# Kernel optimization log

Measured on AMD Instinct MI355X. Metric: run time of the kernel, lower is better.

## Reference

```python
import jax, jax.numpy as jnp
import numpy as np

N, E, B = 50000, 200000, 512
F0, H1, C2, EMB = 78, 10, 128, 128
SEQ, VOCAB, NF, KW = 1000, 26, 32, 8
LOUT = EMB - KW + 1  # 121


def setup_inputs() -> dict:
    key = jax.random.key(0)
    ks = jax.random.split(key, 20)
    nrm = lambda k, s: jax.random.normal(k, s, jnp.float32) * 0.05
    return dict(
        x=jax.random.normal(ks[0], (N, F0), jnp.float32),
        edge_index=jax.random.randint(ks[1], (2, E), 0, N),
        batch=(jnp.arange(N) * B) // N,  # balanced sorted node->graph ids, all segments non-empty
        target=jax.random.randint(ks[2], (B, SEQ), 0, VOCAB),
        W1=nrm(ks[3], (F0, H1 * F0)), a_src1=nrm(ks[4], (H1, F0)), a_dst1=nrm(ks[5], (H1, F0)), b1=jnp.zeros((H1 * F0,), jnp.float32),
        W2=nrm(ks[6], (H1 * F0, C2)), a_src2=nrm(ks[7], (1, C2)), a_dst2=nrm(ks[8], (1, C2)), b2=jnp.zeros((C2,), jnp.float32),
        fc_g1_w=nrm(ks[9], (C2, C2)), fc_g1_b=jnp.zeros((C2,), jnp.float32),
        emb=nrm(ks[10], (VOCAB, EMB)),
        conv_w=nrm(ks[11], (NF, SEQ, KW)), conv_b=jnp.zeros((NF,), jnp.float32),
        fc_xt_w=nrm(ks[12], (NF * LOUT, C2)), fc_xt_b=jnp.zeros((C2,), jnp.float32),
        fc1_w=nrm(ks[13], (2 * C2, 1024)), fc1_b=jnp.zeros((1024,), jnp.float32),
        fc2_w=nrm(ks[14], (1024, 256)), fc2_b=jnp.zeros((256,), jnp.float32),
        out_w=nrm(ks[15], (256, 1)), out_b=jnp.zeros((1,), jnp.float32),
    )


def gat_conv(x, src, dst, W, a_src, a_dst, b, heads):
    # PyG GATConv (eval mode): project, per-edge attn logits, segment softmax over dst, scatter-add
    n = x.shape[0]
    c = W.shape[1] // heads
    h = (x @ W).reshape(n, heads, c)                 # [N,H,C]
    al_s = (h * a_src).sum(-1)                       # [N,H]
    al_d = (h * a_dst).sum(-1)
    al = jax.nn.leaky_relu(al_s[src] + al_d[dst], 0.2)   # [E',H]
    amax = jax.ops.segment_max(al, dst, num_segments=n)
    ex = jnp.exp(al - amax[dst])
    den = jax.ops.segment_sum(ex, dst, num_segments=n)
    alpha = ex / (den[dst] + 1e-16)
    out = jax.ops.segment_sum(h[src] * alpha[:, :, None], dst, num_segments=n)  # [N,H,C]
    return out.reshape(n, heads * c) + b


def reference(x, edge_index, batch, target, W1, a_src1, a_dst1, b1, W2, a_src2, a_dst2, b2,
              fc_g1_w, fc_g1_b, emb, conv_w, conv_b, fc_xt_w, fc_xt_b,
              fc1_w, fc1_b, fc2_w, fc2_b, out_w, out_b):
    n = x.shape[0]
    loops = jnp.arange(n)
    src = jnp.concatenate([edge_index[0], loops])    # add self loops (PyG default)
    dst = jnp.concatenate([edge_index[1], loops])
    h = jax.nn.elu(gat_conv(x, src, dst, W1, a_src1, a_dst1, b1, H1))
    h = jax.nn.relu(gat_conv(h, src, dst, W2, a_src2, a_dst2, b2, 1))
    g = jax.ops.segment_max(h, batch, num_segments=B)            # global max pool per graph
    g = jax.nn.relu(g @ fc_g1_w + fc_g1_b)                       # [B,128]
    e = emb[target]                                              # [B,1000,128]
    conv = jax.lax.conv_general_dilated(e, conv_w, (1,), 'VALID',
                                        dimension_numbers=('NCH', 'OIH', 'NCH'))
    conv = jax.nn.relu(conv + conv_b[None, :, None])             # [B,32,121]
    xt = conv.reshape(B, NF * LOUT) @ fc_xt_w + fc_xt_b          # [B,128]
    xc = jnp.concatenate([g, xt], axis=1)                        # [B,256]
    xc = jax.nn.relu(xc @ fc1_w + fc1_b)
    xc = jax.nn.relu(xc @ fc2_w + fc2_b)
    return xc @ out_w + out_b                                    # [B,1]
```

## Files before the change

kernel.cpp:

```cpp
#include <hip/hip_runtime.h>
#include <hip/hip_bf16.h>

#define N_NODES 50000
#define N_EDGES 200000
#define BGRAPHS 512
#define F0c 78
#define H1c 10
#define HC1 780
#define HSTR 832
#define C2c 128
#define SEQc 1000
#define VOCABc 26
#define NFc 32
#define KWc 8
#define LOUTc 121
#define EMBc 128
#define KX 96
#define KXT 3872
#define KSTEPS2 13

typedef __attribute__((ext_vector_type(8))) short short8;
typedef __attribute__((ext_vector_type(4))) float f32x4;
typedef unsigned short u16;

static constexpr size_t alignup(size_t x) { return (x + 255) & ~size_t(255); }

static constexpr size_t A_HBUF = 0;
static constexpr size_t A_OUT1 = alignup(A_HBUF + size_t(N_NODES)*HSTR*2);
static constexpr size_t A_H2   = alignup(A_OUT1 + size_t(N_NODES)*HSTR*2);
static constexpr size_t A_W2T  = alignup(A_H2   + size_t(N_NODES)*C2c*4);
static constexpr size_t A_ALS1 = alignup(A_W2T  + size_t(C2c)*HSTR*2);
static constexpr size_t A_ALD1 = alignup(A_ALS1 + size_t(N_NODES)*H1c*4);
static constexpr size_t A_ALS2 = alignup(A_ALD1 + size_t(N_NODES)*H1c*4);
static constexpr size_t A_ALD2 = alignup(A_ALS2 + size_t(N_NODES)*4);
static constexpr size_t A_DEG  = alignup(A_ALD2 + size_t(N_NODES)*4);
static constexpr size_t A_OFFS = alignup(A_DEG  + size_t(N_NODES)*4);
static constexpr size_t A_CUR  = alignup(A_OFFS + size_t(N_NODES+1)*4);
static constexpr size_t A_CSRC = alignup(A_CUR  + size_t(N_NODES)*4);
static constexpr size_t A_XC   = alignup(A_CSRC + size_t(N_EDGES+N_NODES)*4);
static constexpr size_t A_Y1   = alignup(A_XC   + size_t(BGRAPHS)*256*4);
static constexpr size_t A_BOFF = alignup(A_Y1   + size_t(BGRAPHS)*1024*4);
static constexpr size_t A_BPAD = alignup(A_BOFF + size_t(BGRAPHS)*(VOCABc+1)*4);
static constexpr size_t A_WXT  = alignup(A_BPAD + size_t(HSTR)*4);
static constexpr size_t A_FXP  = alignup(A_WXT  + size_t(C2c)*KXT*2);
static constexpr size_t A_W1HP = alignup(A_FXP  + size_t(11)*BGRAPHS*C2c*4);
static constexpr size_t A_WSD  = alignup(A_W1HP + size_t(10)*80*96*2);
static constexpr size_t A_END  = alignup(A_WSD  + size_t(2)*H1c*F0c*4);

static constexpr size_t A_HFIN = A_HBUF;
static constexpr size_t A_ORD  = alignup(A_HFIN + size_t(N_NODES)*C2c*4);
static constexpr size_t A_AMAT = alignup(A_ORD  + size_t(BGRAPHS)*SEQc*4);
static constexpr size_t A_CVO  = alignup(A_AMAT + size_t(BGRAPHS)*NFc*VOCABc*KWc*4);
static_assert(A_CVO + size_t(BGRAPHS)*KXT*2 <= size_t(N_NODES)*HSTR*2, "alias A overflow");
static constexpr size_t A_XPAD = A_OUT1;
static_assert(size_t(N_NODES)*KX*2 <= size_t(N_NODES)*HSTR*2, "alias B overflow");

__device__ __forceinline__ float bflo(unsigned u) { return __uint_as_float(u << 16); }
__device__ __forceinline__ float bfhi(unsigned u) { return __uint_as_float(u & 0xffff0000u); }
__device__ __forceinline__ u16 f2bf(float v) {
    __hip_bfloat16 b = __float2bfloat16(v);
    return *(u16*)&b;
}

#define GLOAD16(g, l) __builtin_amdgcn_global_load_lds( \
    (const __attribute__((address_space(1))) void*)(g), \
    (__attribute__((address_space(3))) void*)(l), 16, 0, 0)

__global__ void k_prep(const float* __restrict__ x, const float* __restrict__ W1,
                       const float* __restrict__ W2, const float* __restrict__ b1,
                       const float* __restrict__ fcxt_w,
                       const float* __restrict__ a_src1, const float* __restrict__ a_dst1,
                       __hip_bfloat16* __restrict__ xpad, __hip_bfloat16* __restrict__ w1hp,
                       __hip_bfloat16* __restrict__ w2t, float* __restrict__ bpad,
                       __hip_bfloat16* __restrict__ wxt, float* __restrict__ wsd,
                       int* __restrict__ deg) {
    int i = blockIdx.x*256 + threadIdx.x;
    const int R0 = N_NODES;
    const int R1 = R0 + N_NODES*KX;
    const int R2 = R1 + 10*80*96;
    const int R3 = R2 + C2c*HSTR;
    const int R4 = R3 + HSTR;
    const int R5 = R4 + C2c*KXT;
    const int R6 = R5 + 2*H1c*F0c;
    if (i < R0) {
        deg[i] = 1;
    } else if (i < R1) {
        int t = i - R0; int n = t / KX, c = t - n*KX;
        xpad[t] = __float2bfloat16(c < F0c ? x[(size_t)n*F0c + c] : 0.f);
    } else if (i < R2) {
        int t = i - R1; int hh = t / 7680, rem = t - hh*7680;
        int j = rem / 96, k = rem - j*96;
        w1hp[t] = __float2bfloat16((j < F0c && k < F0c) ? W1[(size_t)k*HC1 + hh*F0c + j] : 0.f);
    } else if (i < R3) {
        int t = i - R2; int c = t / HSTR, p = t - c*HSTR;
        int hh = p / 80, cc = p - hh*80;
        w2t[t] = __float2bfloat16((hh < H1c && cc < F0c) ? W2[(size_t)(hh*F0c + cc)*C2c + c] : 0.f);
    } else if (i < R4) {
        int p = i - R3; int hh = p / 80, cc = p - hh*80;
        bpad[p] = (hh < H1c && cc < F0c) ? b1[hh*F0c + cc] : 0.f;
    } else if (i < R5) {
        int t = i - R4; int c = t / KXT, j = t - c*KXT;
        wxt[t] = __float2bfloat16(fcxt_w[(size_t)j*C2c + c]);
    } else if (i < R6) {
        int t = i - R5; int sd = t / (H1c*F0c), rem = t - sd*(H1c*F0c);
        int hh = rem / F0c, c = rem - hh*F0c;
        const float* a = sd ? a_dst1 : a_src1;
        float v = 0.f;
        for (int j = 0; j < F0c; j++) v += W1[(size_t)c*HC1 + hh*F0c + j] * a[hh*F0c + j];
        wsd[t] = v;
    }
}
#define PREP_TOTAL (N_NODES + N_NODES*KX + 10*80*96 + C2c*HSTR + HSTR + C2c*KXT + 2*H1c*F0c)

__global__ void k_count(const int* __restrict__ ei, int* deg) {
    int i = blockIdx.x*256 + threadIdx.x;
    if (i < N_EDGES) atomicAdd(&deg[ei[N_EDGES + i]], 1);
}
__global__ void k_scan(const int* __restrict__ deg, int* __restrict__ off,
                       int* __restrict__ cur, int n) {
    __shared__ int wsum[16];
    __shared__ int s_carry;
    int tid = threadIdx.x, lane = tid & 63, wid = tid >> 6;
    if (tid == 0) s_carry = 0;
    __syncthreads();
    for (int base = 0; base < n; base += 1024) {
        int i = base + tid;
        int v0 = (i < n) ? deg[i] : 0;
        int v = v0;
        for (int d = 1; d < 64; d <<= 1) { int t = __shfl_up(v, d, 64); if (lane >= d) v += t; }
        if (lane == 63) wsum[wid] = v;
        __syncthreads();
        if (wid == 0) {
            int w = (lane < 16) ? wsum[lane] : 0;
            for (int d = 1; d < 16; d <<= 1) { int t = __shfl_up(w, d, 64); if (lane >= d) w += t; }
            if (lane < 16) wsum[lane] = w;
        }
        __syncthreads();
        int wprev = (wid > 0) ? wsum[wid-1] : 0;
        int carry = s_carry;
        if (i < n) { int o = carry + wprev + (v - v0); off[i] = o; cur[i] = o; }
        __syncthreads();
        if (tid == 0) s_carry = carry + wsum[15];
        __syncthreads();
    }
    if (tid == 0) off[n] = s_carry;
}
__global__ void k_fill(const int* __restrict__ ei, int* cur, int* __restrict__ csrc) {
    int i = blockIdx.x*256 + threadIdx.x;
    if (i < N_EDGES) {
        int s = ei[i], d = ei[N_EDGES + i];
        int p = atomicAdd(&cur[d], 1);
        csrc[p] = s;
    } else if (i < N_EDGES + N_NODES) {
        int n = i - N_EDGES;
        int p = atomicAdd(&cur[n], 1);
        csrc[p] = n;
    }
}
__global__ void k_sortcsr(const int* __restrict__ offs, int* __restrict__ csrc) {
    int n = blockIdx.x*256 + threadIdx.x;
    if (n >= N_NODES) return;
    int s = offs[n], e = offs[n+1];
    for (int i = s + 1; i < e; i++) {
        int v = csrc[i];
        int j = i - 1;
        while (j >= s && csrc[j] > v) { csrc[j+1] = csrc[j]; j--; }
        csrc[j+1] = v;
    }
}

__global__ void k_att1x(const float* __restrict__ x, const float* __restrict__ wsd,
                        float* __restrict__ als, float* __restrict__ ald) {
    int i = blockIdx.x*256 + threadIdx.x;
    if (i >= N_NODES*H1c) return;
    int n = i / H1c, hh = i - n*H1c;
    const float* xr = x + (size_t)n*F0c;
    const float* ws = wsd + hh*F0c;
    const float* wd = wsd + H1c*F0c + hh*F0c;
    float s1 = 0.f, s2 = 0.f;
    for (int c = 0; c < F0c; c++) { float v = xr[c]; s1 += v*ws[c]; s2 += v*wd[c]; }
    als[i] = s1; ald[i] = s2;
}

__global__ void k_agg1x(const unsigned* __restrict__ xpu, const float* __restrict__ als,
                        const float* __restrict__ ald, const int* __restrict__ offs,
                        const int* __restrict__ csrc, unsigned* __restrict__ xaggu) {
    constexpr int H = H1c;
    int dn = blockIdx.x, lane = threadIdx.x;
    int s = offs[dn], e = offs[dn+1], deg = e - s;
    __shared__ float wexp[64*H];
    __shared__ int   ssrc[64];
    __shared__ float ms[H], dinv_s[H];

    if (deg <= 64) {
        if (lane < deg) ssrc[lane] = csrc[s + lane];
        __syncthreads();
        for (int idx = lane; idx < deg*H; idx += 64) {
            int j = idx / H, hh = idx - j*H;
            float al = als[(size_t)ssrc[j]*H + hh] + ald[(size_t)dn*H + hh];
            wexp[idx] = (al >= 0.f) ? al : 0.2f*al;
        }
        __syncthreads();
        if (lane < H) {
            float m = -1e30f;
            for (int j = 0; j < deg; j++) m = fmaxf(m, wexp[j*H + lane]);
            float den = 0.f;
            for (int j = 0; j < deg; j++) den += __expf(wexp[j*H + lane] - m);
            ms[lane] = m; dinv_s[lane] = 1.f/(den + 1e-16f);
        }
        __syncthreads();
        for (int idx = lane; idx < deg*H; idx += 64) {
            int hh = idx % H;
            wexp[idx] = __expf(wexp[idx] - ms[hh]) * dinv_s[hh];
        }
        __syncthreads();
        if (lane < 40) {
            float accL[H], accH[H];
            #pragma unroll
            for (int hh = 0; hh < H; hh++) { accL[hh] = 0.f; accH[hh] = 0.f; }
            int j = 0;
            for (; j + 1 < deg; j += 2) {
                unsigned ua = xpu[(size_t)ssrc[j]*48 + lane];
                unsigned ub = xpu[(size_t)ssrc[j+1]*48 + lane];
                float a0 = bflo(ua), a1 = bfhi(ua), b0 = bflo(ub), b1 = bfhi(ub);
                #pragma unroll
                for (int hh = 0; hh < H; hh++) {
                    float wA = wexp[j*H + hh], wB = wexp[(j+1)*H + hh];
                    accL[hh] += wA*a0 + wB*b0;
                    accH[hh] += wA*a1 + wB*b1;
                }
            }
            if (j < deg) {
                unsigned ua = xpu[(size_t)ssrc[j]*48 + lane];
                float a0 = bflo(ua), a1 = bfhi(ua);
                #pragma unroll
                for (int hh = 0; hh < H; hh++) {
                    float wA = wexp[j*H + hh];
                    accL[hh] += wA*a0;
                    accH[hh] += wA*a1;
                }
            }
            #pragma unroll
            for (int hh = 0; hh < H; hh++) {
                unsigned p = (unsigned)f2bf(accL[hh]) | ((unsigned)f2bf(accH[hh]) << 16);
                xaggu[((size_t)dn*H + hh)*40 + lane] = p;
            }
        }
    } else {
        if (lane < H) {
            float adv = ald[(size_t)dn*H + lane];
            float m = -1e30f;
            for (int j = s; j < e; j++) {
                float al = als[(size_t)csrc[j]*H + lane] + adv;
                al = (al >= 0.f) ? al : 0.2f*al;
                m = fmaxf(m, al);
            }
            float den = 0.f;
            for (int j = s; j < e; j++) {
                float al = als[(size_t)csrc[j]*H + lane] + adv;
                al = (al >= 0.f) ? al : 0.2f*al;
                den += __expf(al - m);
            }
            ms[lane] = m; dinv_s[lane] = 1.f/(den + 1e-16f);
        }
        __syncthreads();
        if (lane < 40) {
            float accL[H], accH[H];
            #pragma unroll
            for (int hh = 0; hh < H; hh++) { accL[hh] = 0.f; accH[hh] = 0.f; }
            for (int j = s; j < e; j++) {
                int sj = csrc[j];
                unsigned ua = xpu[(size_t)sj*48 + lane];
                float a0 = bflo(ua), a1 = bfhi(ua);
                #pragma unroll
                for (int hh = 0; hh < H; hh++) {
                    float al = als[(size_t)sj*H + hh] + ald[(size_t)dn*H + hh];
                    al = (al >= 0.f) ? al : 0.2f*al;
                    float a = __expf(al - ms[hh]) * dinv_s[hh];
                    accL[hh] += a*a0;
                    accH[hh] += a*a1;
                }
            }
            #pragma unroll
            for (int hh = 0; hh < H; hh++) {
                unsigned p = (unsigned)f2bf(accL[hh]) | ((unsigned)f2bf(accH[hh]) << 16);
                xaggu[((size_t)dn*H + hh)*40 + lane] = p;
            }
        }
    }
}

__global__ void k_gemm1h(const short* __restrict__ xagg, const short* __restrict__ w1hp,
                         const float* __restrict__ bpad, u16* __restrict__ out1) {
    int wave = threadIdx.x >> 6, lane = threadIdx.x & 63;
    int m16 = lane & 15, quad = lane >> 4;
    int hh = blockIdx.y;
    int r0 = blockIdx.x*64 + wave*16;
    int rowc = min(r0 + m16, N_NODES-1);
    const short8* arow = (const short8*)(xagg + ((size_t)rowc*H1c + hh)*80);
    f32x4 acc[5];
    #pragma unroll
    for (int ct = 0; ct < 5; ct++) acc[ct] = (f32x4){0.f,0.f,0.f,0.f};
    #pragma unroll
    for (int kt = 0; kt < 3; kt++) {
        short8 af = arow[kt*4 + quad];
        #pragma unroll
        for (int ct = 0; ct < 5; ct++) {
            const short8* brow = (const short8*)(w1hp + (size_t)(hh*80 + ct*16 + m16)*96);
            short8 bf = brow[kt*4 + quad];
            acc[ct] = __builtin_amdgcn_mfma_f32_16x16x32_bf16(af, bf, acc[ct], 0, 0, 0);
        }
    }
    #pragma unroll
    for (int ct = 0; ct < 5; ct++) {
        int col = ct*16 + m16;
        float bv = bpad[hh*80 + col];
        #pragma unroll
        for (int r = 0; r < 4; r++) {
            int orow = r0 + quad*4 + r;
            if (orow < N_NODES) {
                float v = acc[ct][r] + bv;
                v = (v > 0.f) ? v : (__expf(v) - 1.f);
                out1[(size_t)orow*HSTR + hh*80 + col] = f2bf(v);
            }
        }
    }
    if (blockIdx.y == 0) {
        int rr = blockIdx.x*64 + (threadIdx.x >> 2);
        if (rr < N_NODES) {
            short8 z = (short8){0,0,0,0,0,0,0,0};
            *(short8*)&out1[(size_t)rr*HSTR + 800 + (threadIdx.x & 3)*8] = z;
        }
    }
}

__global__ void __launch_bounds__(256, 2)
k_gemm2_mfma(const short* __restrict__ A, const short* __restrict__ Bt,
             const float* __restrict__ a_src2, const float* __restrict__ a_dst2,
             float* __restrict__ Cout, float* __restrict__ als2,
             float* __restrict__ ald2) {
    __shared__ __attribute__((aligned(16))) short As[2][128*64];
    __shared__ __attribute__((aligned(16))) short Bs[2][128*64];
    int tid = threadIdx.x;
    int wave = tid >> 6, lane = tid & 63;
    int m16 = lane & 15, quad = lane >> 4;
    int blockrow = blockIdx.x * 128;

    size_t aoff[4], boff[4];
    #pragma unroll
    for (int i = 0; i < 4; i++) {
        int c = wave*256 + i*64 + lane;
        int row = c >> 3;
        int cb  = (c & 7) << 4;
        int srcb = cb ^ ((row & 7) << 4);
        int ga = blockrow + row; if (ga > N_NODES-1) ga = N_NODES-1;
        aoff[i] = (size_t)ga  * (HSTR*2) + srcb;
        boff[i] = (size_t)row * (HSTR*2) + srcb;
    }

    f32x4 acc[2][8];
    #pragma unroll
    for (int wr = 0; wr < 2; wr++)
        #pragma unroll
        for (int ct = 0; ct < 8; ct++) acc[wr][ct] = (f32x4){0.f,0.f,0.f,0.f};

    #pragma unroll
    for (int i = 0; i < 4; i++) {
        GLOAD16((const char*)A  + aoff[i], &As[0][(wave*256 + i*64)*8]);
        GLOAD16((const char*)Bt + boff[i], &Bs[0][(wave*256 + i*64)*8]);
    }
    __syncthreads();

    int cur = 0;
    int S = (m16 & 7) << 4;
    for (int s = 0; s < KSTEPS2; s++) {
        if (s + 1 < KSTEPS2) {
            size_t kb = (size_t)(s + 1) * 128;
            #pragma unroll
            for (int i = 0; i < 4; i++) {
                GLOAD16((const char*)A  + aoff[i] + kb, &As[cur^1][(wave*256 + i*64)*8]);
                GLOAD16((const char*)Bt + boff[i] + kb, &Bs[cur^1][(wave*256 + i*64)*8]);
            }
        }
        const char* asBase = (const char*)&As[cur][0];
        const char* bsBase = (const char*)&Bs[cur][0];
        #pragma unroll
        for (int kk = 0; kk < 2; kk++) {
            int kb = (kk*64 + quad*16) ^ S;
            short8 af[2];
            #pragma unroll
            for (int wr = 0; wr < 2; wr++) {
                int row = wave*32 + wr*16 + m16;
                af[wr] = *(const short8*)(asBase + row*128 + kb);
            }
            #pragma unroll
            for (int ct = 0; ct < 8; ct++) {
                int col = ct*16 + m16;
                short8 bfv = *(const short8*)(bsBase + col*128 + kb);
                acc[0][ct] = __builtin_amdgcn_mfma_f32_16x16x32_bf16(af[0], bfv, acc[0][ct], 0, 0, 0);
                acc[1][ct] = __builtin_amdgcn_mfma_f32_16x16x32_bf16(af[1], bfv, acc[1][ct], 0, 0, 0);
            }
        }
        __syncthreads();
        cur ^= 1;
    }

    float asv[8], adv[8];
    #pragma unroll
    for (int ct = 0; ct < 8; ct++) { asv[ct] = a_src2[ct*16 + m16]; adv[ct] = a_dst2[ct*16 + m16]; }
    #pragma unroll
    for (int wr = 0; wr < 2; wr++) {
        int rowbase = blockrow + wave*32 + wr*16;
        #pragma unroll
        for (int ct = 0; ct < 8; ct++) {
            int col = ct*16 + m16;
            #pragma unroll
            for (int r = 0; r < 4; r++) {
                int orow = rowbase + quad*4 + r;
                if (orow < N_NODES) Cout[(size_t)orow*C2c + col] = acc[wr][ct][r];
            }
        }
        #pragma unroll
        for (int r = 0; r < 4; r++) {
            float s1 = 0.f, s2 = 0.f;
            #pragma unroll
            for (int ct = 0; ct < 8; ct++) { s1 += acc[wr][ct][r]*asv[ct]; s2 += acc[wr][ct][r]*adv[ct]; }
            #pragma unroll
            for (int d = 1; d < 16; d <<= 1) { s1 += __shfl_xor(s1, d, 64); s2 += __shfl_xor(s2, d, 64); }
            int orow = rowbase + quad*4 + r;
            if (m16 == 0 && orow < N_NODES) { als2[orow] = s1; ald2[orow] = s2; }
        }
    }
}

__global__ void k_agg2(const float* __restrict__ h2, const float* __restrict__ als,
                       const float* __restrict__ ald, const int* __restrict__ offs,
                       const int* __restrict__ csrc, const float* __restrict__ b2,
                       float* __restrict__ out) {
    int dn = blockIdx.x, lane = threadIdx.x;
    int s = offs[dn], e = offs[dn+1], deg = e - s;
    __shared__ float wexp[128];
    __shared__ int ssrc[128];

    if (deg <= 128) {
        float adv = ald[dn];
        for (int j = lane; j < deg; j += 64) {
            int sj = csrc[s + j];
            ssrc[j] = sj;
            float al = als[sj] + adv;
            wexp[j] = (al >= 0.f) ? al : 0.2f*al;
        }
        __syncthreads();
        float m = -1e30f;
        for (int j = lane; j < deg; j += 64) m = fmaxf(m, wexp[j]);
        #pragma unroll
        for (int d = 32; d > 0; d >>= 1) m = fmaxf(m, __shfl_xor(m, d, 64));
        __syncthreads();
        float den = 0.f;
        for (int j = lane; j < deg; j += 64) {
            float ex = __expf(wexp[j] - m);
            wexp[j] = ex;
            den += ex;
        }
        #pragma unroll
        for (int d = 32; d > 0; d >>= 1) den += __shfl_xor(den, d, 64);
        float dinv = 1.f/(den + 1e-16f);
        __syncthreads();
        float2 acc = {0.f, 0.f};
        for (int j = 0; j < deg; j++) {
            float alpha = wexp[j] * dinv;
            float2 v = ((const float2*)(h2 + (size_t)ssrc[j]*C2c))[lane];
            acc.x += alpha*v.x; acc.y += alpha*v.y;
        }
        float2 o;
        o.x = fmaxf(acc.x + b2[2*lane], 0.f);
        o.y = fmaxf(acc.y + b2[2*lane+1], 0.f);
        ((float2*)(out + (size_t)dn*C2c))[lane] = o;
    } else {
        __shared__ float sm[2];
        if (lane == 0) {
            float adv = ald[dn];
            float m = -1e30f;
            for (int j = s; j < e; j++) {
                float al = als[csrc[j]] + adv;
                al = (al >= 0.f) ? al : 0.2f*al;
                m = fmaxf(m, al);
            }
            float den = 0.f;
            for (int j = s; j < e; j++) {
                float al = als[csrc[j]] + adv;
                al = (al >= 0.f) ? al : 0.2f*al;
                den += __expf(al - m);
            }
            sm[0] = m; sm[1] = 1.f/(den + 1e-16f);
        }
        __syncthreads();
        float m = sm[0], dinv = sm[1], adv = ald[dn];
        float2 acc = {0.f, 0.f};
        for (int j = s; j < e; j++) {
            int sj = csrc[j];
            float al = als[sj] + adv;
            al = (al >= 0.f) ? al : 0.2f*al;
            float alpha = __expf(al - m) * dinv;
            float2 v = ((const float2*)(h2 + (size_t)sj*C2c))[lane];
            acc.x += alpha*v.x; acc.y += alpha*v.y;
        }
        float2 o;
        o.x = fmaxf(acc.x + b2[2*lane], 0.f);
        o.y = fmaxf(acc.y + b2[2*lane+1], 0.f);
        ((float2*)(out + (size_t)dn*C2c))[lane] = o;
    }
}

__global__ void k_poolfcg(const float* __restrict__ hf, const int* __restrict__ batch,
                          const float* __restrict__ W, const float* __restrict__ bias,
                          float* __restrict__ xc) {
    int b = blockIdx.x, tid = threadIdx.x;
    __shared__ int se[2];
    __shared__ float gs[C2c];
    if (tid < 2) {
        int key = b + tid;
        int lo = 0, hi = N_NODES;
        while (lo < hi) { int mid = (lo+hi) >> 1; if (batch[mid] < key) lo = mid+1; else hi = mid; }
        se[tid] = lo;
    }
    __syncthreads();
    int s = se[0], e = se[1];
    float m = -1e30f;
    for (int n = s; n < e; n++) m = fmaxf(m, hf[(size_t)n*C2c + tid]);
    gs[tid] = m;
    __syncthreads();
    float acc = bias[tid];
    for (int k = 0; k < C2c; k++) acc += gs[k] * W[k*C2c + tid];
    xc[b*256 + tid] = fmaxf(acc, 0.f);
}

__global__ void k_bucket(const int* __restrict__ target, int* __restrict__ ordered,
                         int* __restrict__ boff) {
    int b = blockIdx.x, tid = threadIdx.x;
    __shared__ unsigned char tg[SEQc];
    __shared__ u16 cnt[VOCABc][256];
    __shared__ int offs_s[VOCABc+1];
    __shared__ int tot[VOCABc];
    for (int i = tid; i < VOCABc*256; i += 256) ((u16*)cnt)[i] = 0;
    __syncthreads();
    int i0 = tid*4;
    #pragma unroll
    for (int k = 0; k < 4; k++) {
        int i = i0 + k;
        if (i < SEQc) {
            int t = target[(size_t)b*SEQc + i];
            tg[i] = (unsigned char)t;
            cnt[t][tid]++;
        }
    }
    __syncthreads();
    if (tid < VOCABc) {
        int run = 0;
        for (int c = 0; c < 256; c++) {
            int v = cnt[tid][c];
            cnt[tid][c] = (u16)run;
            run += v;
        }
        tot[tid] = run;
    }
    __syncthreads();
    if (tid == 0) {
        offs_s[0] = 0;
        for (int v = 0; v < VOCABc; v++) offs_s[v+1] = offs_s[v] + tot[v];
    }
    __syncthreads();
    if (tid < VOCABc+1) boff[b*(VOCABc+1) + tid] = offs_s[tid];
    #pragma unroll
    for (int k = 0; k < 4; k++) {
        int i = i0 + k;
        if (i < SEQc) {
            int t = tg[i];
            int r = cnt[t][tid]++;
            ordered[(size_t)b*SEQc + offs_s[t] + r] = i;
        }
    }
}
__global__ void k_buildA(const float* __restrict__ convw, const int* __restrict__ ordered,
                         const int* __restrict__ boff, float* __restrict__ Amat) {
    int t = blockIdx.x, b = blockIdx.y;
    int tid = threadIdx.x;
    int o = tid >> 3, k = tid & 7;
    int s = boff[b*(VOCABc+1) + t], e = boff[b*(VOCABc+1) + t + 1];
    __shared__ int sidx[256];
    float acc = 0.f;
    for (int base = s; base < e; base += 256) {
        int m = min(256, e - base);
        __syncthreads();
        if (tid < m) sidx[tid] = ordered[(size_t)b*SEQc + base + tid];
        __syncthreads();
        #pragma unroll 4
        for (int j = 0; j < m; j++) {
            acc += convw[((size_t)o*SEQc + sidx[j])*KWc + k];
        }
    }
    Amat[(((size_t)b*NFc + o)*VOCABc + t)*KWc + k] = acc;
}
__global__ void __launch_bounds__(128, 4)
k_conv(const float* __restrict__ Amat, const float* __restrict__ emb,
       const float* __restrict__ convb, u16* __restrict__ convout) {
    int b = blockIdx.x, og = blockIdx.y;
    int tid = threadIdx.x;
    __shared__ float embs[VOCABc*EMBc];
    __shared__ float arow[4*VOCABc*KWc];
    for (int i = tid; i < VOCABc*EMBc; i += 128) embs[i] = emb[i];
    for (int i = tid; i < 4*VOCABc*KWc; i += 128)
        arow[i] = Amat[((size_t)b*NFc + og*4)*(VOCABc*KWc) + i];
    __syncthreads();
    if (tid < LOUTc) {
        float a0 = convb[og*4+0], a1 = convb[og*4+1], a2 = convb[og*4+2], a3 = convb[og*4+3];
        for (int t = 0; t < VOCABc; t++) {
            #pragma unroll
            for (int k = 0; k < KWc; k++) {
                float ev = embs[t*EMBc + tid + k];
                a0 += arow[0*(VOCABc*KWc) + t*KWc + k] * ev;
                a1 += arow[1*(VOCABc*KWc) + t*KWc + k] * ev;
                a2 += arow[2*(VOCABc*KWc) + t*KWc + k] * ev;
                a3 += arow[3*(VOCABc*KWc) + t*KWc + k] * ev;
            }
        }
        size_t base = (size_t)b*KXT + (og*4)*LOUTc + tid;
        convout[base            ] = f2bf(fmaxf(a0, 0.f));
        convout[base +   LOUTc  ] = f2bf(fmaxf(a1, 0.f));
        convout[base + 2*LOUTc  ] = f2bf(fmaxf(a2, 0.f));
        convout[base + 3*LOUTc  ] = f2bf(fmaxf(a3, 0.f));
    }
}
__global__ void k_fcxt_mfma(const short* __restrict__ cvo, const short* __restrict__ wxt,
                            float* __restrict__ fxp) {
    int wave = threadIdx.x >> 6, lane = threadIdx.x & 63;
    int m16 = lane & 15, quad = lane >> 4;
    int r0 = blockIdx.x*64 + wave*16;
    int kt0 = blockIdx.y*11;
    const short8* arow = (const short8*)(cvo + (size_t)(r0 + m16)*KXT);
    f32x4 acc[8];
    #pragma unroll
    for (int ct = 0; ct < 8; ct++) acc[ct] = (f32x4){0.f,0.f,0.f,0.f};
    for (int kt = kt0; kt < kt0 + 11; kt++) {
        short8 af = arow[kt*4 + quad];
        #pragma unroll
        for (int ct = 0; ct < 8; ct++) {
            const short8* brow = (const short8*)(wxt + (size_t)(ct*16 + m16)*KXT);
            short8 bf = brow[kt*4 + quad];
            acc[ct] = __builtin_amdgcn_mfma_f32_16x16x32_bf16(af, bf, acc[ct], 0, 0, 0);
        }
    }
    #pragma unroll
    for (int ct = 0; ct < 8; ct++) {
        int col = ct*16 + m16;
        #pragma unroll
        for (int r = 0; r < 4; r++) {
            int row = r0 + quad*4 + r;
            fxp[((size_t)blockIdx.y*BGRAPHS + row)*C2c + col] = acc[ct][r];
        }
    }
}

__global__ void k_fc1(const float* __restrict__ xc, const float* __restrict__ fxp,
                      const float* __restrict__ fcxt_b, const float* __restrict__ W,
                      const float* __restrict__ bias, float* __restrict__ y1) {
    int b = blockIdx.x, tid = threadIdx.x;
    __shared__ float xs[256];
    if (tid < 128) {
        xs[tid] = xc[b*256 + tid];
    } else {
        int col = tid - 128;
        float s = fcxt_b[col];
        #pragma unroll
        for (int q = 0; q < 11; q++) s += fxp[((size_t)q*BGRAPHS + b)*C2c + col];
        xs[tid] = s;
    }
    __syncthreads();
    float a0 = bias[tid], a1 = bias[tid+256], a2 = bias[tid+512], a3 = bias[tid+768];
    for (int k = 0; k < 256; k++) {
        float xk = xs[k];
        const float* wr = W + (size_t)k*1024;
        a0 += xk*wr[tid]; a1 += xk*wr[tid+256]; a2 += xk*wr[tid+512]; a3 += xk*wr[tid+768];
    }
    y1[(size_t)b*1024 + tid      ] = fmaxf(a0, 0.f);
    y1[(size_t)b*1024 + tid + 256] = fmaxf(a1, 0.f);
    y1[(size_t)b*1024 + tid + 512] = fmaxf(a2, 0.f);
    y1[(size_t)b*1024 + tid + 768] = fmaxf(a3, 0.f);
}
__global__ void k_fc2out(const float* __restrict__ y1, const float* __restrict__ W,
                         const float* __restrict__ bias, const float* __restrict__ ow,
                         const float* __restrict__ ob, float* __restrict__ out) {
    int b = blockIdx.x, tid = threadIdx.x;
    int lane = tid & 63, wid = tid >> 6;
    __shared__ float ys[1024];
    __shared__ float wsum[4];
    for (int i = tid; i < 1024; i += 256) ys[i] = y1[(size_t)b*1024 + i];
    __syncthreads();
    float acc = bias[tid];
    for (int k = 0; k < 1024; k++) acc += ys[k] * W[(size_t)k*256 + tid];
    float v = fmaxf(acc, 0.f) * ow[tid];
    #pragma unroll
    for (int d = 32; d > 0; d >>= 1) v += __shfl_xor(v, d, 64);
    if (lane == 0) wsum[wid] = v;
    __syncthreads();
    if (tid == 0) out[b] = wsum[0] + wsum[1] + wsum[2] + wsum[3] + ob[0];
}

extern "C" void kernel_launch(void* const* d_in, const int* in_sizes, int n_in,
                              void* d_out, int out_size, void* d_ws, size_t ws_size,
                              hipStream_t stream) {
    (void)in_sizes; (void)n_in; (void)out_size;
    if (ws_size < A_END) return;

    const float* x       = (const float*)d_in[0];
    const int*   ei      = (const int*)  d_in[1];
    const int*   batch   = (const int*)  d_in[2];
    const int*   target  = (const int*)  d_in[3];
    const float* W1      = (const float*)d_in[4];
    const float* a_src1  = (const float*)d_in[5];
    const float* a_dst1  = (const float*)d_in[6];
    const float* b1      = (const float*)d_in[7];
    const float* W2      = (const float*)d_in[8];
    const float* a_src2  = (const float*)d_in[9];
    const float* a_dst2  = (const float*)d_in[10];
    const float* b2      = (const float*)d_in[11];
    const float* fcg_w   = (const float*)d_in[12];
    const float* fcg_b   = (const float*)d_in[13];
    const float* emb     = (const float*)d_in[14];
    const float* conv_w  = (const float*)d_in[15];
    const float* conv_b  = (const float*)d_in[16];
    const float* fcxt_w  = (const float*)d_in[17];
    const float* fcxt_b  = (const float*)d_in[18];
    const float* fc1_w   = (const float*)d_in[19];
    const float* fc1_b   = (const float*)d_in[20];
    const float* fc2_w   = (const float*)d_in[21];
    const float* fc2_b   = (const float*)d_in[22];
    const float* out_w   = (const float*)d_in[23];
    const float* out_b   = (const float*)d_in[24];

    char* wsb = (char*)d_ws;
    u16*   xagg  = (u16*)  (wsb + A_HBUF);
    u16*   out1  = (u16*)  (wsb + A_OUT1);
    float* h2    = (float*)(wsb + A_H2);
    __hip_bfloat16* w2t = (__hip_bfloat16*)(wsb + A_W2T);
    float* als1  = (float*)(wsb + A_ALS1);
    float* ald1  = (float*)(wsb + A_ALD1);
    float* als2  = (float*)(wsb + A_ALS2);
    float* ald2  = (float*)(wsb + A_ALD2);
    int*   deg   = (int*)  (wsb + A_DEG);
    int*   offs  = (int*)  (wsb + A_OFFS);
    int*   cur   = (int*)  (wsb + A_CUR);
    int*   csrc  = (int*)  (wsb + A_CSRC);
    float* xc    = (float*)(wsb + A_XC);
    float* y1    = (float*)(wsb + A_Y1);
    int*   boff  = (int*)  (wsb + A_BOFF);
    float* bpad  = (float*)(wsb + A_BPAD);
    __hip_bfloat16* wxt  = (__hip_bfloat16*)(wsb + A_WXT);
    float* fxp   = (float*)(wsb + A_FXP);
    __hip_bfloat16* w1hp = (__hip_bfloat16*)(wsb + A_W1HP);
    float* wsd   = (float*)(wsb + A_WSD);
    float* hfin  = (float*)(wsb + A_HFIN);
    int*   ord   = (int*)  (wsb + A_ORD);
    float* Amat  = (float*)(wsb + A_AMAT);
    u16*   cvo   = (u16*)  (wsb + A_CVO);
    __hip_bfloat16* xpad = (__hip_bfloat16*)(wsb + A_XPAD);

    k_prep<<<(PREP_TOTAL+255)/256, 256, 0, stream>>>(x, W1, W2, b1, fcxt_w, a_src1, a_dst1,
                                                     xpad, w1hp, w2t, bpad, wxt, wsd, deg);
    k_count  <<<(N_EDGES+255)/256, 256, 0, stream>>>(ei, deg);
    k_scan   <<<1, 1024, 0, stream>>>(deg, offs, cur, N_NODES);
    k_fill   <<<(N_EDGES+N_NODES+255)/256, 256, 0, stream>>>(ei, cur, csrc);
    k_sortcsr<<<(N_NODES+255)/256, 256, 0, stream>>>(offs, csrc);

    k_att1x<<<(N_NODES*H1c+255)/256, 256, 0, stream>>>(x, wsd, als1, ald1);
    k_agg1x<<<N_NODES, 64, 0, stream>>>((const unsigned*)xpad, als1, ald1, offs, csrc,
                                        (unsigned*)xagg);
    k_gemm1h<<<dim3((N_NODES+63)/64, H1c), 256, 0, stream>>>((const short*)xagg,
                                                             (const short*)w1hp, bpad, out1);

    k_gemm2_mfma<<<(N_NODES+127)/128, 256, 0, stream>>>((const short*)out1, (const short*)w2t,
                                                        a_src2, a_dst2, h2, als2, ald2);
    k_agg2<<<N_NODES, 64, 0, stream>>>(h2, als2, ald2, offs, csrc, b2, hfin);

    k_poolfcg<<<BGRAPHS, 128, 0, stream>>>(hfin, batch, fcg_w, fcg_b, xc);

    k_bucket<<<BGRAPHS, 256, 0, stream>>>(target, ord, boff);
    k_buildA<<<dim3(VOCABc, BGRAPHS), 256, 0, stream>>>(conv_w, ord, boff, Amat);
    k_conv  <<<dim3(BGRAPHS, 8), 128, 0, stream>>>(Amat, emb, conv_b, cvo);
    k_fcxt_mfma<<<dim3(BGRAPHS/64, 11), 256, 0, stream>>>((const short*)cvo, (const short*)wxt, fxp);

    k_fc1<<<BGRAPHS, 256, 0, stream>>>(xc, fxp, fcxt_b, fc1_w, fc1_b, y1);
    k_fc2out<<<BGRAPHS, 256, 0, stream>>>(y1, fc2_w, fc2_b, out_w, out_b, (float*)d_out);
}
```

Measured before the change: 595.3 us.

## Compute conv A-matrix via one-hot bf16 MFMA GEMM with hi/lo split weights

Replaces the per-graph token bucketing and gather-sum that built the per-vocab conv coefficient matrix with a dense GEMM. A one-hot matrix [B*VOCAB, 1024] is multiplied against the conv weights, which are stored transposed as bf16 hi and lo halves to keep near-fp32 accuracy. The GEMM runs on MFMA with double-buffered LDS loads. This removes the irregular gather loops but adds roughly 27 MB of one-hot writes and reads, plus twice the MFMA work for the hi/lo split.

```diff
diff --git a/kernel.cpp b/kernel.cpp
--- a/kernel.cpp
+++ b/kernel.cpp
@@ -18,6 +18,8 @@
 #define KX 96
 #define KXT 3872
 #define KSTEPS2 13
+#define MROWS 13312
+#define KM 1024
 
 typedef __attribute__((ext_vector_type(8))) short short8;
 typedef __attribute__((ext_vector_type(4))) float f32x4;
@@ -45,13 +47,14 @@
 static constexpr size_t A_FXP  = alignup(A_WXT  + size_t(C2c)*KXT*2);
 static constexpr size_t A_W1HP = alignup(A_FXP  + size_t(11)*BGRAPHS*C2c*4);
 static constexpr size_t A_WSD  = alignup(A_W1HP + size_t(10)*80*96*2);
-static constexpr size_t A_END  = alignup(A_WSD  + size_t(2)*H1c*F0c*4);
+static constexpr size_t A_CWT  = alignup(A_WSD  + size_t(2)*H1c*F0c*4);
+static constexpr size_t A_END  = alignup(A_CWT  + size_t(2)*256*KM*2);
 
 static constexpr size_t A_HFIN = A_HBUF;
-static constexpr size_t A_ORD  = alignup(A_HFIN + size_t(N_NODES)*C2c*4);
-static constexpr size_t A_AMAT = alignup(A_ORD  + size_t(BGRAPHS)*SEQc*4);
-static constexpr size_t A_CVO  = alignup(A_AMAT + size_t(BGRAPHS)*NFc*VOCABc*KWc*4);
-static_assert(A_CVO + size_t(BGRAPHS)*KXT*2 <= size_t(N_NODES)*HSTR*2, "alias A overflow");
+static constexpr size_t A_AMAT = alignup(A_HFIN + size_t(N_NODES)*C2c*4);
+static constexpr size_t A_CVO  = alignup(A_AMAT + size_t(MROWS)*256*4);
+static constexpr size_t A_M    = alignup(A_CVO  + size_t(BGRAPHS)*KXT*2);
+static_assert(A_M + size_t(MROWS)*KM*2 <= size_t(N_NODES)*HSTR*2, "alias A overflow");
 static constexpr size_t A_XPAD = A_OUT1;
 static_assert(size_t(N_NODES)*KX*2 <= size_t(N_NODES)*HSTR*2, "alias B overflow");
 
@@ -68,12 +71,12 @@
 
 __global__ void k_prep(const float* __restrict__ x, const float* __restrict__ W1,
                        const float* __restrict__ W2, const float* __restrict__ b1,
-                       const float* __restrict__ fcxt_w,
+                       const float* __restrict__ fcxt_w, const float* __restrict__ conv_w,
                        const float* __restrict__ a_src1, const float* __restrict__ a_dst1,
                        __hip_bfloat16* __restrict__ xpad, __hip_bfloat16* __restrict__ w1hp,
                        __hip_bfloat16* __restrict__ w2t, float* __restrict__ bpad,
                        __hip_bfloat16* __restrict__ wxt, float* __restrict__ wsd,
-                       int* __restrict__ deg) {
+                       u16* __restrict__ cwt, int* __restrict__ deg) {
     int i = blockIdx.x*256 + threadIdx.x;
     const int R0 = N_NODES;
     const int R1 = R0 + N_NODES*KX;
@@ -82,6 +85,7 @@
     const int R4 = R3 + HSTR;
     const int R5 = R4 + C2c*KXT;
     const int R6 = R5 + 2*H1c*F0c;
+    const int R7 = R6 + 256*KM;
     if (i < R0) {
         deg[i] = 1;
     } else if (i < R1) {
@@ -108,9 +112,17 @@
         float v = 0.f;
         for (int j = 0; j < F0c; j++) v += W1[(size_t)c*HC1 + hh*F0c + j] * a[hh*F0c + j];
         wsd[t] = v;
-    }
-}
-#define PREP_TOTAL (N_NODES + N_NODES*KX + 10*80*96 + C2c*HSTR + HSTR + C2c*KXT + 2*H1c*F0c)
+    } else if (i < R7) {
+        int t = i - R6; int col = t >> 10, ii = t & (KM-1);
+        int o = col >> 3, k = col & 7;
+        float v = (ii < SEQc) ? conv_w[((size_t)o*SEQc + ii)*KWc + k] : 0.f;
+        u16 h = f2bf(v);
+        float hv = __uint_as_float((unsigned)h << 16);
+        cwt[(size_t)col*KM + ii] = h;
+        cwt[(size_t)256*KM + (size_t)col*KM + ii] = f2bf(v - hv);
+    }
+}
+#define PREP_TOTAL (N_NODES + N_NODES*KX + 10*80*96 + C2c*HSTR + HSTR + C2c*KXT + 2*H1c*F0c + 256*KM)
 
 __global__ void k_count(const int* __restrict__ ei, int* deg) {
     int i = blockIdx.x*256 + threadIdx.x;
@@ -535,82 +547,124 @@
     xc[b*256 + tid] = fmaxf(acc, 0.f);
 }
 
-__global__ void k_bucket(const int* __restrict__ target, int* __restrict__ ordered,
-                         int* __restrict__ boff) {
+__global__ void k_buildM(const int* __restrict__ target, u16* __restrict__ Mm) {
     int b = blockIdx.x, tid = threadIdx.x;
-    __shared__ unsigned char tg[SEQc];
-    __shared__ u16 cnt[VOCABc][256];
-    __shared__ int offs_s[VOCABc+1];
-    __shared__ int tot[VOCABc];
-    for (int i = tid; i < VOCABc*256; i += 256) ((u16*)cnt)[i] = 0;
-    __syncthreads();
-    int i0 = tid*4;
-    #pragma unroll
-    for (int k = 0; k < 4; k++) {
-        int i = i0 + k;
-        if (i < SEQc) {
-            int t = target[(size_t)b*SEQc + i];
-            tg[i] = (unsigned char)t;
-            cnt[t][tid]++;
-        }
-    }
-    __syncthreads();
-    if (tid < VOCABc) {
-        int run = 0;
-        for (int c = 0; c < 256; c++) {
-            int v = cnt[tid][c];
-            cnt[tid][c] = (u16)run;
-            run += v;
-        }
-        tot[tid] = run;
-    }
-    __syncthreads();
-    if (tid == 0) {
-        offs_s[0] = 0;
-        for (int v = 0; v < VOCABc; v++) offs_s[v+1] = offs_s[v] + tot[v];
-    }
-    __syncthreads();
-    if (tid < VOCABc+1) boff[b*(VOCABc+1) + tid] = offs_s[tid];
-    #pragma unroll
-    for (int k = 0; k < 4; k++) {
-        int i = i0 + k;
-        if (i < SEQc) {
-            int t = tg[i];
-            int r = cnt[t][tid]++;
-            ordered[(size_t)b*SEQc + offs_s[t] + r] = i;
-        }
-    }
-}
-__global__ void k_buildA(const float* __restrict__ convw, const int* __restrict__ ordered,
-                         const int* __restrict__ boff, float* __restrict__ Amat) {
-    int t = blockIdx.x, b = blockIdx.y;
+    short8 z = (short8){0,0,0,0,0,0,0,0};
+    short8* base = (short8*)(Mm + (size_t)b*VOCABc*KM);
+    for (int i = tid; i < VOCABc*KM/8; i += 256) base[i] = z;
+    __syncthreads();
+    for (int i = tid; i < SEQc; i += 256) {
+        int t = target[(size_t)b*SEQc + i];
+        Mm[((size_t)b*VOCABc + t)*KM + i] = (u16)0x3F80;
+    }
+}
+
+__global__ void __launch_bounds__(256, 1)
+k_amat_mfma(const short* __restrict__ Mm, const short* __restrict__ cwt,
+            float* __restrict__ A2) {
+    __shared__ __attribute__((aligned(16))) short As[2][128*64];
+    __shared__ __attribute__((aligned(16))) short Bh[2][128*64];
+    __shared__ __attribute__((aligned(16))) short Bl[2][128*64];
     int tid = threadIdx.x;
-    int o = tid >> 3, k = tid & 7;
-    int s = boff[b*(VOCABc+1) + t], e = boff[b*(VOCABc+1) + t + 1];
-    __shared__ int sidx[256];
-    float acc = 0.f;
-    for (int base = s; base < e; base += 256) {
-        int m = min(256, e - base);
-        __syncthreads();
-        if (tid < m) sidx[tid] = ordered[(size_t)b*SEQc + base + tid];
-        __syncthreads();
-        #pragma unroll 4
-        for (int j = 0; j < m; j++) {
-            acc += convw[((size_t)o*SEQc + sidx[j])*KWc + k];
-        }
-    }
-    Amat[(((size_t)b*NFc + o)*VOCABc + t)*KWc + k] = acc;
-}
+    int wave = tid >> 6, lane = tid & 63;
+    int m16 = lane & 15, quad = lane >> 4;
+    int blockrow = blockIdx.x * 128;
+    int colbase  = blockIdx.y * 128;
+
+    size_t aoff[4], bo[4];
+    #pragma unroll
+    for (int i = 0; i < 4; i++) {
+        int c = wave*256 + i*64 + lane;
+        int row = c >> 3;
+        int cb  = (c & 7) << 4;
+        int srcb = cb ^ ((row & 7) << 4);
+        aoff[i] = (size_t)(blockrow + row) * (KM*2) + srcb;
+        bo[i]   = (size_t)(colbase  + row) * (KM*2) + srcb;
+    }
+    const char* hbase = (const char*)cwt;
+    const char* lbase = (const char*)(cwt + (size_t)256*KM);
+
+    f32x4 acc[2][8];
+    #pragma unroll
+    for (int wr = 0; wr < 2; wr++)
+        #pragma unroll
+        for (int ct = 0; ct < 8; ct++) acc[wr][ct] = (f32x4){0.f,0.f,0.f,0.f};
+
+    #pragma unroll
+    for (int i = 0; i < 4; i++) {
+        GLOAD16((const char*)Mm + aoff[i], &As[0][(wave*256 + i*64)*8]);
+        GLOAD16(hbase + bo[i],             &Bh[0][(wave*256 + i*64)*8]);
+        GLOAD16(lbase + bo[i],             &Bl[0][(wave*256 + i*64)*8]);
+    }
+    __syncthreads();
+
+    int cur = 0;
+    int S = (m16 & 7) << 4;
+    for (int s = 0; s < KM/64; s++) {
+        if (s + 1 < KM/64) {
+            size_t kb = (size_t)(s + 1) * 128;
+            #pragma unroll
+            for (int i = 0; i < 4; i++) {
+                GLOAD16((const char*)Mm + aoff[i] + kb, &As[cur^1][(wave*256 + i*64)*8]);
+                GLOAD16(hbase + bo[i] + kb,             &Bh[cur^1][(wave*256 + i*64)*8]);
+                GLOAD16(lbase + bo[i] + kb,             &Bl[cur^1][(wave*256 + i*64)*8]);
+            }
+        }
+        const char* asBase = (const char*)&As[cur][0];
+        const char* bhBase = (const char*)&Bh[cur][0];
+        const char* blBase = (const char*)&Bl[cur][0];
+        #pragma unroll
+        for (int kk = 0; kk < 2; kk++) {
+            int kb2 = (kk*64 + quad*16) ^ S;
+            short8 af[2];
+            #pragma unroll
+            for (int wr = 0; wr < 2; wr++) {
+                int row = wave*32 + wr*16 + m16;
+                af[wr] = *(const short8*)(asBase + row*128 + kb2);
+            }
+            #pragma unroll
+            for (int ct = 0; ct < 8; ct++) {
+                int col = ct*16 + m16;
+                short8 bhv = *(const short8*)(bhBase + col*128 + kb2);
+                short8 blv = *(const short8*)(blBase + col*128 + kb2);
+                acc[0][ct] = __builtin_amdgcn_mfma_f32_16x16x32_bf16(af[0], bhv, acc[0][ct], 0, 0, 0);
+                acc[1][ct] = __builtin_amdgcn_mfma_f32_16x16x32_bf16(af[1], bhv, acc[1][ct], 0, 0, 0);
+                acc[0][ct] = __builtin_amdgcn_mfma_f32_16x16x32_bf16(af[0], blv, acc[0][ct], 0, 0, 0);
+                acc[1][ct] = __builtin_amdgcn_mfma_f32_16x16x32_bf16(af[1], blv, acc[1][ct], 0, 0, 0);
+            }
+        }
+        __syncthreads();
+        cur ^= 1;
+    }
+
+    #pragma unroll
+    for (int wr = 0; wr < 2; wr++) {
+        int rowbase = blockrow + wave*32 + wr*16 + quad*4;
+        #pragma unroll
+        for (int ct = 0; ct < 8; ct++) {
+            int col = colbase + ct*16 + m16;
+            #pragma unroll
+            for (int r = 0; r < 4; r++) {
+                A2[(size_t)(rowbase + r)*256 + col] = acc[wr][ct][r];
+            }
+        }
+    }
+}
+
 __global__ void __launch_bounds__(128, 4)
-k_conv(const float* __restrict__ Amat, const float* __restrict__ emb,
+k_conv(const float* __restrict__ A2, const float* __restrict__ emb,
        const float* __restrict__ convb, u16* __restrict__ convout) {
     int b = blockIdx.x, og = blockIdx.y;
     int tid = threadIdx.x;
     __shared__ float embs[VOCABc*EMBc];
     __shared__ float arow[4*VOCABc*KWc];
     for (int i = tid; i < VOCABc*EMBc; i += 128) embs[i] = emb[i];
-    for (int i = tid; i < 4*VOCABc*KWc; i += 128)
-        arow[i] = Amat[((size_t)b*NFc + og*4)*(VOCABc*KWc) + i];
+    for (int i = tid; i < 4*VOCABc*KWc; i += 128) {
+        int o2 = i / (VOCABc*KWc);
+        int rem = i - o2*(VOCABc*KWc);
+        int t = rem >> 3, k = rem & 7;
+        arow[i] = A2[((size_t)b*VOCABc + t)*256 + (og*4 + o2)*8 + k];
+    }
     __syncthreads();
     if (tid < LOUTc) {
         float a0 = convb[og*4+0], a1 = convb[og*4+1], a2 = convb[og*4+2], a3 = convb[og*4+3];
@@ -753,20 +807,21 @@
     int*   csrc  = (int*)  (wsb + A_CSRC);
     float* xc    = (float*)(wsb + A_XC);
     float* y1    = (float*)(wsb + A_Y1);
-    int*   boff  = (int*)  (wsb + A_BOFF);
     float* bpad  = (float*)(wsb + A_BPAD);
     __hip_bfloat16* wxt  = (__hip_bfloat16*)(wsb + A_WXT);
     float* fxp   = (float*)(wsb + A_FXP);
     __hip_bfloat16* w1hp = (__hip_bfloat16*)(wsb + A_W1HP);
     float* wsd   = (float*)(wsb + A_WSD);
+    u16*   cwt   = (u16*)  (wsb + A_CWT);
     float* hfin  = (float*)(wsb + A_HFIN);
-    int*   ord   = (int*)  (wsb + A_ORD);
-    float* Amat  = (float*)(wsb + A_AMAT);
+    float* Amat2 = (float*)(wsb + A_AMAT);
     u16*   cvo   = (u16*)  (wsb + A_CVO);
+    u16*   Mm    = (u16*)  (wsb + A_M);
     __hip_bfloat16* xpad = (__hip_bfloat16*)(wsb + A_XPAD);
 
-    k_prep<<<(PREP_TOTAL+255)/256, 256, 0, stream>>>(x, W1, W2, b1, fcxt_w, a_src1, a_dst1,
-                                                     xpad, w1hp, w2t, bpad, wxt, wsd, deg);
+    k_prep<<<(PREP_TOTAL+255)/256, 256, 0, stream>>>(x, W1, W2, b1, fcxt_w, conv_w,
+                                                     a_src1, a_dst1,
+                                                     xpad, w1hp, w2t, bpad, wxt, wsd, cwt, deg);
     k_count  <<<(N_EDGES+255)/256, 256, 0, stream>>>(ei, deg);
     k_scan   <<<1, 1024, 0, stream>>>(deg, offs, cur, N_NODES);
     k_fill   <<<(N_EDGES+N_NODES+255)/256, 256, 0, stream>>>(ei, cur, csrc);
@@ -778,15 +833,17 @@
     k_gemm1h<<<dim3((N_NODES+63)/64, H1c), 256, 0, stream>>>((const short*)xagg,
                                                              (const short*)w1hp, bpad, out1);
 
+    k_buildM<<<BGRAPHS, 256, 0, stream>>>(target, Mm);
+
     k_gemm2_mfma<<<(N_NODES+127)/128, 256, 0, stream>>>((const short*)out1, (const short*)w2t,
                                                         a_src2, a_dst2, h2, als2, ald2);
     k_agg2<<<N_NODES, 64, 0, stream>>>(h2, als2, ald2, offs, csrc, b2, hfin);
 
     k_poolfcg<<<BGRAPHS, 128, 0, stream>>>(hfin, batch, fcg_w, fcg_b, xc);
 
-    k_bucket<<<BGRAPHS, 256, 0, stream>>>(target, ord, boff);
-    k_buildA<<<dim3(VOCABc, BGRAPHS), 256, 0, stream>>>(conv_w, ord, boff, Amat);
-    k_conv  <<<dim3(BGRAPHS, 8), 128, 0, stream>>>(Amat, emb, conv_b, cvo);
+    k_amat_mfma<<<dim3(MROWS/128, 2), 256, 0, stream>>>((const short*)Mm, (const short*)cwt,
+                                                        Amat2);
+    k_conv  <<<dim3(BGRAPHS, 8), 128, 0, stream>>>(Amat2, emb, conv_b, cvo);
     k_fcxt_mfma<<<dim3(BGRAPHS/64, 11), 256, 0, stream>>>((const short*)cvo, (const short*)wxt, fxp);
 
     k_fc1<<<BGRAPHS, 256, 0, stream>>>(xc, fxp, fcxt_b, fc1_w, fc1_b, y1);
```

Result: faster. 566.2 us (-4.9%).
